# Optimization experiments

Hardware: AMD Instinct MI355X
Metric: run time of the kernel (lower is better)

Reference implementation:

```python
import jax, jax.numpy as jnp
import numpy as np
from jax import lax

# mamba-130m-style config
B, L = 2, 1024          # batch, seq_len
D = 768                 # hidden_size
E = 1536                # intermediate (expand=2)
N = 16                  # ssm state size
R = 48                  # time_step_rank = ceil(D/16)
K = 4                   # conv kernel
NL = 4                  # num layers
NC = 5                  # num classes
EPS = 1e-5


def setup_inputs() -> dict:
    key = jax.random.key(0)
    ks = jax.random.split(key, 10)
    s = 0.02
    return {
        "x": jax.random.normal(ks[0], (B, L, 12), dtype=jnp.float32),
        "proj_w": jax.random.normal(ks[1], (D, 12)) * s,
        "proj_b": jnp.zeros((D,), jnp.float32),
        "norm_w": jnp.ones((NL, D), jnp.float32),
        "in_w": jax.random.normal(ks[2], (NL, 2 * E, D)) * s,
        "conv_w": jax.random.normal(ks[3], (NL, E, K)) * s,
        "conv_b": jnp.zeros((NL, E), jnp.float32),
        "xproj_w": jax.random.normal(ks[4], (NL, R + 2 * N, E)) * s,
        "dt_w": jax.random.normal(ks[5], (NL, E, R)) * s,
        "dt_b": jnp.full((NL, E), -4.0, jnp.float32),  # softplus(-4) ~ small dt
        "A_log": jnp.tile(jnp.log(jnp.arange(1, N + 1, dtype=jnp.float32))[None, None, :], (NL, E, 1)),
        "D_param": jnp.ones((NL, E), jnp.float32),
        "out_w": jax.random.normal(ks[6], (NL, D, E)) * s,
        "fnorm_w": jnp.ones((D,), jnp.float32),
        "cls_w": jax.random.normal(ks[7], (NC, D)) * s,
        "cls_b": jnp.zeros((NC,), jnp.float32),
    }


def _rmsnorm(x, w):
    var = jnp.mean(x * x, axis=-1, keepdims=True)
    return x * lax.rsqrt(var + EPS) * w


def _causal_conv(u, w, b):
    # u: [B,L,E], w: [E,K] depthwise causal conv, left-pad K-1
    up = jnp.pad(u, ((0, 0), (K - 1, 0), (0, 0)))
    y = b
    for k in range(K):
        y = y + w[:, k] * up[:, k:k + L, :]
    return y


def _selective_scan(u, dt, A, Bm, Cm, Dp):
    # u, dt: [B,L,E]; Bm, Cm: [B,L,N]; A: [E,N]; Dp: [E]
    def step(h, inp):
        u_t, dt_t, B_t, C_t = inp  # [B,E],[B,E],[B,N],[B,N]
        dA = jnp.exp(dt_t[:, :, None] * A)                      # [B,E,N]
        h = h * dA + dt_t[:, :, None] * B_t[:, None, :] * u_t[:, :, None]
        y = jnp.einsum('ben,bn->be', h, C_t)
        return h, y

    h0 = jnp.zeros((u.shape[0], E, N), u.dtype)
    _, ys = lax.scan(step, h0,
                     (u.transpose(1, 0, 2), dt.transpose(1, 0, 2),
                      Bm.transpose(1, 0, 2), Cm.transpose(1, 0, 2)))
    return ys.transpose(1, 0, 2) + u * Dp


def reference(x, proj_w, proj_b, norm_w, in_w, conv_w, conv_b, xproj_w,
              dt_w, dt_b, A_log, D_param, out_w, fnorm_w, cls_w, cls_b):
    h = x @ proj_w.T + proj_b                                     # [B,L,D]
    for i in range(NL):
        res = h
        hn = _rmsnorm(h, norm_w[i])
        proj = hn @ in_w[i].T                                     # [B,L,2E]
        u, gate = proj[..., :E], proj[..., E:]
        u = jax.nn.silu(_causal_conv(u, conv_w[i], conv_b[i]))    # [B,L,E]
        xdbc = u @ xproj_w[i].T                                   # [B,L,R+2N]
        dt_r = xdbc[..., :R]
        Bm = xdbc[..., R:R + N]
        Cm = xdbc[..., R + N:]
        dt = jax.nn.softplus(dt_r @ dt_w[i].T + dt_b[i])          # [B,L,E]
        A = -jnp.exp(A_log[i])                                    # [E,N]
        y = _selective_scan(u, dt, A, Bm, Cm, D_param[i])
        y = y * jax.nn.silu(gate)
        h = res + y @ out_w[i].T
    h = _rmsnorm(h, fnorm_w)
    pooled = jnp.mean(h, axis=1)                                  # AdaptiveAvgPool1d(1)
    return pooled @ cls_w.T + cls_b                               # [B,NC]
```

## Files before the change

### kernel.cpp

```cpp
#include <hip/hip_runtime.h>

constexpr int B_  = 2;
constexpr int L_  = 1024;
constexpr int D_  = 768;
constexpr int E_  = 1536;
constexpr int N_  = 16;
constexpr int R_  = 48;
constexpr int NL_ = 4;
constexpr int NC_ = 5;
constexpr int M_  = B_ * L_;
constexpr int E2_ = 2 * E_;
constexpr int XD_ = R_ + 2 * N_;
constexpr float EPS_ = 1e-5f;

constexpr int NCH_ = 16;
constexpr int CL_  = L_ / NCH_;
constexpr int TS_  = 32;
constexpr int KS_  = 8;
constexpr int XSL_ = E_ / KS_;
constexpr int USTR_ = 200;

typedef __attribute__((ext_vector_type(8))) short bf16x8;
typedef __attribute__((ext_vector_type(4))) float f32x4;
typedef const __attribute__((address_space(1))) void* gas_t;
typedef __attribute__((address_space(3))) void* las_t;

__device__ __forceinline__ float sigm(float x) { return 1.0f / (1.0f + __expf(-x)); }
__device__ __forceinline__ float softplusf(float x) { return x > 20.0f ? x : log1pf(__expf(x)); }
__device__ __forceinline__ ushort f2b(float f) {
  union { float f; unsigned u; } v; v.f = f;
  unsigned r = (v.u + 0x7fffu + ((v.u >> 16) & 1u)) >> 16;
  return (ushort)r;
}
__device__ __forceinline__ float b2f(ushort u) {
  union { unsigned u; float f; } v; v.u = ((unsigned)u) << 16;
  return v.f;
}
__device__ __forceinline__ float b2f_lo(unsigned p) {
  union { unsigned u; float f; } v; v.u = p << 16;
  return v.f;
}
__device__ __forceinline__ float b2f_hi(unsigned p) {
  union { unsigned u; float f; } v; v.u = p & 0xffff0000u;
  return v.f;
}

template <int CTRL>
__device__ __forceinline__ float dpp_add(float x) {
  int yi = __builtin_amdgcn_update_dpp(0, __builtin_bit_cast(int, x), CTRL, 0xf, 0xf, false);
  return x + __builtin_bit_cast(float, yi);
}
__device__ __forceinline__ float row_sum16(float x) {
  x = dpp_add<0x121>(x);
  x = dpp_add<0x122>(x);
  x = dpp_add<0x124>(x);
  x = dpp_add<0x128>(x);
  return x;
}

__device__ __forceinline__ float block_sum(float v, float* sm) {
  #pragma unroll
  for (int o = 32; o > 0; o >>= 1) v += __shfl_xor(v, o);
  if ((threadIdx.x & 63) == 0) sm[threadIdx.x >> 6] = v;
  __syncthreads();
  return sm[0] + sm[1] + sm[2] + sm[3];
}

constexpr int WS1_ = NL_ * E2_ * D_;
constexpr int WS2_ = NL_ * D_ * E_;
constexpr int WS3_ = NL_ * XD_ * E_;
constexpr int WS4_ = NL_ * E_ * 64;
__global__ __launch_bounds__(256) void k_wprep(const float* __restrict__ in_w, const float* __restrict__ out_w,
                                               const float* __restrict__ xw, const float* __restrict__ dw,
                                               ushort* __restrict__ in_wb, ushort* __restrict__ out_wb,
                                               ushort* __restrict__ xwb, ushort* __restrict__ dtwb) {
  int i = (blockIdx.x * 256 + threadIdx.x) * 4;
  if (i < WS1_) {
    float4 v = *(const float4*)(in_w + i);
    *(ushort4*)(in_wb + i) = make_ushort4(f2b(v.x), f2b(v.y), f2b(v.z), f2b(v.w));
  } else if (i < WS1_ + WS2_) {
    int j = i - WS1_;
    float4 v = *(const float4*)(out_w + j);
    *(ushort4*)(out_wb + j) = make_ushort4(f2b(v.x), f2b(v.y), f2b(v.z), f2b(v.w));
  } else if (i < WS1_ + WS2_ + WS3_) {
    int j = i - WS1_ - WS2_;
    float4 v = *(const float4*)(xw + j);
    *(ushort4*)(xwb + j) = make_ushort4(f2b(v.x), f2b(v.y), f2b(v.z), f2b(v.w));
  } else if (i < WS1_ + WS2_ + WS3_ + WS4_) {
    int j = i - WS1_ - WS2_ - WS3_;
    int k = j & 63, e = j >> 6;
    ushort4 o;
    o.x = (k + 0 < R_) ? f2b(dw[e * R_ + k + 0]) : (ushort)0;
    o.y = (k + 1 < R_) ? f2b(dw[e * R_ + k + 1]) : (ushort)0;
    o.z = (k + 2 < R_) ? f2b(dw[e * R_ + k + 2]) : (ushort)0;
    o.w = (k + 3 < R_) ? f2b(dw[e * R_ + k + 3]) : (ushort)0;
    *(ushort4*)(dtwb + j) = o;
  }
}

__global__ __launch_bounds__(256) void k_proj(const float* __restrict__ x, const float* __restrict__ pw,
                                              const float* __restrict__ pb, float* __restrict__ h) {
  __shared__ float xs[12];
  int m = blockIdx.y;
  int d = blockIdx.x * 256 + threadIdx.x;
  if (threadIdx.x < 12) xs[threadIdx.x] = x[m * 12 + threadIdx.x];
  __syncthreads();
  float acc = pb[d];
  #pragma unroll
  for (int j = 0; j < 12; j++) acc = fmaf(xs[j], pw[d * 12 + j], acc);
  h[(size_t)m * D_ + d] = acc;
}

__global__ __launch_bounds__(256) void k_rmsnorm_bf(const float* __restrict__ h, const float* __restrict__ w,
                                                    ushort* __restrict__ hn) {
  __shared__ float sm[4];
  int m = blockIdx.x, tid = threadIdx.x;
  const float* row = h + (size_t)m * D_;
  float v0 = row[tid], v1 = row[tid + 256], v2 = row[tid + 512];
  float s = block_sum(v0 * v0 + v1 * v1 + v2 * v2, sm);
  float sc = rsqrtf(s * (1.0f / D_) + EPS_);
  ushort* o = hn + (size_t)m * D_;
  o[tid]       = f2b(v0 * sc * w[tid]);
  o[tid + 256] = f2b(v1 * sc * w[tid + 256]);
  o[tid + 512] = f2b(v2 * sc * w[tid + 512]);
}

template <int BM, int BN, int MODE>
__global__ __launch_bounds__(256) void k_gemm_bf(const ushort* __restrict__ A, const ushort* __restrict__ Bw,
                                                 void* __restrict__ Cv, const float* __restrict__ res,
                                                 int Kd, int Nd) {
  constexpr int AM = BM / 32, BNF = BN / 32;
  __shared__ ushort sA[BM * 32];
  __shared__ ushort sB[BN * 32];
  const int tid = threadIdx.x;
  const int wave = tid >> 6, lane = tid & 63;
  const int q = lane >> 4, r = lane & 15;
  const int wm = wave >> 1, wn = wave & 1;
  const int m0 = blockIdx.y * BM, n0 = blockIdx.x * BN;
  f32x4 acc[AM][BNF] = {};

  for (int k0 = 0; k0 < Kd; k0 += 32) {
    #pragma unroll
    for (int j = 0; j < BM / 64; j++) {
      int i = j * 256 + tid;
      const ushort* gp = A + (size_t)(m0 + (i >> 2)) * Kd + k0 + ((i & 3) << 3);
      __builtin_amdgcn_global_load_lds((gas_t)gp, (las_t)(sA + ((j * 256 + wave * 64) << 3)), 16, 0, 0);
    }
    #pragma unroll
    for (int j = 0; j < BN / 64; j++) {
      int i = j * 256 + tid;
      const ushort* gp = Bw + (size_t)(n0 + (i >> 2)) * Kd + k0 + ((i & 3) << 3);
      __builtin_amdgcn_global_load_lds((gas_t)gp, (las_t)(sB + ((j * 256 + wave * 64) << 3)), 16, 0, 0);
    }
    __syncthreads();
    bf16x8 af[AM], bfv[BNF];
    #pragma unroll
    for (int mi = 0; mi < AM; mi++)
      af[mi] = *(const bf16x8*)&sA[(wm * (BM / 2) + mi * 16 + r) * 32 + q * 8];
    #pragma unroll
    for (int nj = 0; nj < BNF; nj++)
      bfv[nj] = *(const bf16x8*)&sB[(wn * (BN / 2) + nj * 16 + r) * 32 + q * 8];
    #pragma unroll
    for (int mi = 0; mi < AM; mi++)
      #pragma unroll
      for (int nj = 0; nj < BNF; nj++)
        acc[mi][nj] = __builtin_amdgcn_mfma_f32_16x16x32_bf16(af[mi], bfv[nj], acc[mi][nj], 0, 0, 0);
    __syncthreads();
  }
  #pragma unroll
  for (int mi = 0; mi < AM; mi++) {
    #pragma unroll
    for (int nj = 0; nj < BNF; nj++) {
      int col = n0 + wn * (BN / 2) + nj * 16 + r;
      #pragma unroll
      for (int rg = 0; rg < 4; rg++) {
        int row = m0 + wm * (BM / 2) + mi * 16 + q * 4 + rg;
        size_t off = (size_t)row * Nd + col;
        float v = acc[mi][nj][rg];
        if (MODE == 4) {
          if (col >= (Nd >> 1)) v = v * sigm(v);
          ((ushort*)Cv)[off] = f2b(v);
        } else if (MODE == 6) {
          ((ushort*)Cv)[off] = f2b(softplusf(v + res[col]));
        } else {
          if (MODE == 1) v += res[off];
          ((float*)Cv)[off] = v;
        }
      }
    }
  }
}

__global__ __launch_bounds__(256) void k_gemm_xc(const ushort* __restrict__ proj, const float* __restrict__ cw,
                                                 const float* __restrict__ cb, const ushort* __restrict__ Bw,
                                                 ushort* __restrict__ ub16, float* __restrict__ part) {
  __shared__ ushort sU[64 * USTR_];
  __shared__ ushort sB[80 * USTR_];
  const int tid = threadIdx.x;
  const int wave = tid >> 6, lane = tid & 63;
  const int q = lane >> 4, r = lane & 15;
  const int m0 = blockIdx.x * 64;
  const int kbeg = blockIdx.y * XSL_;

  for (int i = tid; i < 80 * (XSL_ / 8); i += 256) {
    int row = i / (XSL_ / 8), seg = i % (XSL_ / 8);
    bf16x8 v = *(const bf16x8*)(Bw + (size_t)row * E_ + kbeg + seg * 8);
    *(bf16x8*)&sB[row * USTR_ + seg * 8] = v;
  }

  for (int i = tid; i < 64 * (XSL_ / 4); i += 256) {
    int row = i / (XSL_ / 4), e4i = i % (XSL_ / 4);
    int e = kbeg + e4i * 4;
    int m = m0 + row;
    int t = m & (L_ - 1);
    float4 w0 = *(const float4*)(cw + (e + 0) * 4);
    float4 w1 = *(const float4*)(cw + (e + 1) * 4);
    float4 w2 = *(const float4*)(cw + (e + 2) * 4);
    float4 w3 = *(const float4*)(cw + (e + 3) * 4);
    float wv[4][4] = {{w0.x, w0.y, w0.z, w0.w}, {w1.x, w1.y, w1.z, w1.w},
                      {w2.x, w2.y, w2.z, w2.w}, {w3.x, w3.y, w3.z, w3.w}};
    float4 bb = *(const float4*)(cb + e);
    float acc[4] = {bb.x, bb.y, bb.z, bb.w};
    #pragma unroll
    for (int k = 0; k < 4; k++) {
      int tt = t + k - 3;
      if (tt >= 0) {
        uint2 p = *(const uint2*)(proj + (size_t)(m + k - 3) * E2_ + e);
        acc[0] = fmaf(wv[0][k], b2f_lo(p.x), acc[0]);
        acc[1] = fmaf(wv[1][k], b2f_hi(p.x), acc[1]);
        acc[2] = fmaf(wv[2][k], b2f_lo(p.y), acc[2]);
        acc[3] = fmaf(wv[3][k], b2f_hi(p.y), acc[3]);
      }
    }
    float u0 = acc[0] * sigm(acc[0]), u1 = acc[1] * sigm(acc[1]);
    float u2 = acc[2] * sigm(acc[2]), u3 = acc[3] * sigm(acc[3]);
    uint2 uo;
    uo.x = (unsigned)f2b(u0) | ((unsigned)f2b(u1) << 16);
    uo.y = (unsigned)f2b(u2) | ((unsigned)f2b(u3) << 16);
    *(uint2*)(ub16 + (size_t)m * E_ + e) = uo;
    *(uint2*)&sU[row * USTR_ + e4i * 4] = uo;
  }
  __syncthreads();

  f32x4 acc[5] = {};
  #pragma unroll
  for (int k0 = 0; k0 < XSL_ / 32; k0++) {
    bf16x8 af = *(const bf16x8*)&sU[(wave * 16 + r) * USTR_ + k0 * 32 + q * 8];
    #pragma unroll
    for (int nj = 0; nj < 5; nj++) {
      bf16x8 bfv = *(const bf16x8*)&sB[(nj * 16 + r) * USTR_ + k0 * 32 + q * 8];
      acc[nj] = __builtin_amdgcn_mfma_f32_16x16x32_bf16(af, bfv, acc[nj], 0, 0, 0);
    }
  }
  float* pp = part + (size_t)blockIdx.y * M_ * XD_;
  #pragma unroll
  for (int nj = 0; nj < 5; nj++) {
    int col = nj * 16 + r;
    #pragma unroll
    for (int rg = 0; rg < 4; rg++) {
      int row = m0 + wave * 16 + q * 4 + rg;
      pp[(size_t)row * XD_ + col] = acc[nj][rg];
    }
  }
}

__global__ __launch_bounds__(256) void k_xfin(const float* __restrict__ part, float* __restrict__ xdbc,
                                              ushort* __restrict__ xb) {
  int i = blockIdx.x * 256 + threadIdx.x;
  int m = i / XD_, col = i - m * XD_;
  float s = 0.0f;
  #pragma unroll
  for (int ks = 0; ks < KS_; ks++) s += part[(size_t)ks * M_ * XD_ + i];
  xdbc[i] = s;
  if (col < R_) xb[(size_t)m * 64 + col] = f2b(s);
  else if (col < 64) xb[(size_t)m * 64 + col] = 0;
}

__global__ __launch_bounds__(256) void k_scanA(const ushort* __restrict__ u, const ushort* __restrict__ dtb,
                                               const float* __restrict__ xdbc, const float* __restrict__ A_log,
                                               float* __restrict__ Pst, float* __restrict__ Sst) {
  __shared__ float2 s_dtu[2][TS_][16];
  __shared__ float  s_b [2][TS_][16];
  const int tid = threadIdx.x;
  const int e0 = blockIdx.x << 4;
  const int b  = blockIdx.y;
  const int c  = blockIdx.z;
  const int n  = tid & 15, el = tid >> 4;
  const int e  = e0 + el;
  const float A = -__expf(A_log[e * N_ + n]);
  const int se = tid & 15, st = tid >> 4;

  float r_b[2];
  ushort r_dt[2], r_u[2];
  auto issue = [&](int s) {
    int t0 = c * CL_ + s * TS_;
    #pragma unroll
    for (int j = 0; j < 2; j++) {
      size_t m = (size_t)(b * L_ + t0 + j * 16 + st);
      r_dt[j] = dtb[m * E_ + e0 + se];
      r_u[j]  = u[m * E_ + e0 + se];
    }
    #pragma unroll
    for (int j = 0; j < 2; j++) {
      int idx = j * 256 + tid;
      r_b[j] = xdbc[(size_t)(b * L_ + t0 + (idx >> 4)) * XD_ + R_ + (idx & 15)];
    }
  };
  auto commit = [&](int pb) {
    #pragma unroll
    for (int j = 0; j < 2; j++) {
      int t = j * 16 + st;
      float dtv = b2f(r_dt[j]);
      s_dtu[pb][t][se] = make_float2(dtv, dtv * b2f(r_u[j]));
    }
    #pragma unroll
    for (int j = 0; j < 2; j++) {
      int idx = j * 256 + tid;
      s_b[pb][idx >> 4][idx & 15] = r_b[j];
    }
  };

  issue(0);
  commit(0);
  float hs = 0.0f, pp = 1.0f;
  constexpr int NS = CL_ / TS_;
  for (int s = 0; s < NS; s++) {
    __syncthreads();
    if (s + 1 < NS) issue(s + 1);
    const int pb = s & 1;
    #pragma unroll
    for (int t = 0; t < TS_; t++) {
      float2 dtu = s_dtu[pb][t][el];
      float bv   = s_b[pb][t][n];
      float dA = __expf(dtu.x * A);
      hs = fmaf(hs, dA, dtu.y * bv);
      pp *= dA;
    }
    if (s + 1 < NS) commit((s + 1) & 1);
  }
  size_t o = (((size_t)(b * NCH_ + c) * E_) + e) * N_ + n;
  Pst[o] = pp;
  Sst[o] = hs;
}

__global__ __launch_bounds__(256) void k_scanC(const ushort* __restrict__ u, const ushort* __restrict__ dtb,
                                               const float* __restrict__ xdbc, const ushort* __restrict__ proj,
                                               const float* __restrict__ A_log, const float* __restrict__ Dp,
                                               const float* __restrict__ Pst, const float* __restrict__ Sst,
                                               ushort* __restrict__ y) {
  __shared__ float2 s_dtu[2][TS_][16];
  __shared__ float2 s_bc [2][TS_][16];
  __shared__ float2 s_og [2][TS_][16];
  const int tid = threadIdx.x;
  const int e0 = blockIdx.x << 4;
  const int b  = blockIdx.y;
  const int c  = blockIdx.z;
  const int n  = tid & 15, el = tid >> 4;
  const int e  = e0 + el;
  const float A = -__expf(A_log[e * N_ + n]);
  const int se = tid & 15, st = tid >> 4;
  const float Dv = Dp[e0 + se];

  float r_bc[4];
  ushort r_dt[2], r_u[2], r_g[2];
  auto issue = [&](int s) {
    int t0 = c * CL_ + s * TS_;
    #pragma unroll
    for (int j = 0; j < 2; j++) {
      size_t m = (size_t)(b * L_ + t0 + j * 16 + st);
      r_dt[j] = dtb[m * E_ + e0 + se];
      r_u[j]  = u[m * E_ + e0 + se];
      r_g[j]  = proj[m * E2_ + E_ + e0 + se];
    }
    #pragma unroll
    for (int j = 0; j < 4; j++) {
      int idx = j * 256 + tid;
      r_bc[j] = xdbc[(size_t)(b * L_ + t0 + (idx >> 5)) * XD_ + R_ + (idx & 31)];
    }
  };
  auto commit = [&](int pb) {
    #pragma unroll
    for (int j = 0; j < 2; j++) {
      int t = j * 16 + st;
      float dtv = b2f(r_dt[j]);
      float uf = b2f(r_u[j]);
      s_dtu[pb][t][se] = make_float2(dtv, dtv * uf);
      s_og[pb][t][se] = make_float2(uf * Dv, b2f(r_g[j]));
    }
    #pragma unroll
    for (int j = 0; j < 4; j++) {
      int idx = j * 256 + tid;
      int t = idx >> 5, col = idx & 31;
      ((float*)&s_bc[pb][t][0])[((col & 15) << 1) + (col >> 4)] = r_bc[j];
    }
  };

  issue(0);
  float hs = 0.0f;
  for (int cc = 0; cc < c; cc++) {
    size_t o = (((size_t)(b * NCH_ + cc) * E_) + e) * N_ + n;
    hs = fmaf(Pst[o], hs, Sst[o]);
  }
  commit(0);
  constexpr int NS = CL_ / TS_;
  for (int s = 0; s < NS; s++) {
    __syncthreads();
    if (s + 1 < NS) issue(s + 1);
    const int pb = s & 1;
    const int mbase = b * L_ + c * CL_ + s * TS_;
    #pragma unroll
    for (int t = 0; t < TS_; t++) {
      float2 dtu = s_dtu[pb][t][el];
      float2 bc  = s_bc[pb][t][n];
      float dA = __expf(dtu.x * A);
      hs = fmaf(hs, dA, dtu.y * bc.x);
      float p = row_sum16(hs * bc.y);
      if (n == 0) {
        float2 og = s_og[pb][t][el];
        y[(size_t)(mbase + t) * E_ + e] = f2b((p + og.x) * og.y);
      }
    }
    if (s + 1 < NS) commit((s + 1) & 1);
  }
}

__global__ __launch_bounds__(256) void k_rowscale(const float* __restrict__ h, float* __restrict__ rs) {
  __shared__ float sm[4];
  int m = blockIdx.x, tid = threadIdx.x;
  const float* row = h + (size_t)m * D_;
  float v0 = row[tid], v1 = row[tid + 256], v2 = row[tid + 512];
  float s = block_sum(v0 * v0 + v1 * v1 + v2 * v2, sm);
  if (tid == 0) rs[m] = rsqrtf(s * (1.0f / D_) + EPS_);
}

__global__ __launch_bounds__(256) void k_pool(const float* __restrict__ h, const float* __restrict__ rs,
                                              const float* __restrict__ fw, float* __restrict__ pooled) {
  int d = blockIdx.x * 256 + threadIdx.x;
  int t0 = blockIdx.y * 128;
  int b = blockIdx.z;
  float acc = 0.0f;
  for (int t = t0; t < t0 + 128; t++) {
    int m = b * L_ + t;
    acc = fmaf(h[(size_t)m * D_ + d], rs[m], acc);
  }
  atomicAdd(&pooled[b * D_ + d], acc * fw[d] * (1.0f / L_));
}

__global__ __launch_bounds__(256) void k_logits(const float* __restrict__ pooled, const float* __restrict__ cw,
                                                const float* __restrict__ cb, float* __restrict__ out) {
  int wv = threadIdx.x >> 6, ln = threadIdx.x & 63;
  for (int p = wv; p < B_ * NC_; p += 4) {
    int b = p / NC_, c = p % NC_;
    float s = 0.0f;
    for (int d = ln; d < D_; d += 64) s = fmaf(pooled[b * D_ + d], cw[c * D_ + d], s);
    #pragma unroll
    for (int o = 32; o > 0; o >>= 1) s += __shfl_xor(s, o);
    if (ln == 0) out[p] = s + cb[c];
  }
}

extern "C" void kernel_launch(void* const* d_in, const int* in_sizes, int n_in,
                              void* d_out, int out_size, void* d_ws, size_t ws_size,
                              hipStream_t stream) {
  const float* x       = (const float*)d_in[0];
  const float* proj_w  = (const float*)d_in[1];
  const float* proj_b  = (const float*)d_in[2];
  const float* norm_w  = (const float*)d_in[3];
  const float* in_w    = (const float*)d_in[4];
  const float* conv_w  = (const float*)d_in[5];
  const float* conv_b  = (const float*)d_in[6];
  const float* xproj_w = (const float*)d_in[7];
  const float* dt_w    = (const float*)d_in[8];
  const float* dt_b    = (const float*)d_in[9];
  const float* A_log   = (const float*)d_in[10];
  const float* D_param = (const float*)d_in[11];
  const float* out_w   = (const float*)d_in[12];
  const float* fnorm_w = (const float*)d_in[13];
  const float* cls_w   = (const float*)d_in[14];
  const float* cls_b   = (const float*)d_in[15];
  float* out = (float*)d_out;

  float* h      = (float*)d_ws;
  float* xdbc   = h + (size_t)M_ * D_;
  float* rsb    = xdbc + (size_t)M_ * XD_;
  float* pooled = rsb + M_;
  float* Pst    = pooled + B_ * D_;
  float* Sst    = Pst + (size_t)B_ * NCH_ * E_ * N_;
  float* xpart  = Sst + (size_t)B_ * NCH_ * E_ * N_;
  ushort* proj_bf = (ushort*)(xpart + (size_t)KS_ * M_ * XD_);
  ushort* hn_bf   = proj_bf + (size_t)M_ * E2_;
  ushort* y_bf    = hn_bf + (size_t)M_ * D_;
  ushort* ub_bf   = y_bf + (size_t)M_ * E_;
  ushort* dt_bf   = ub_bf + (size_t)M_ * E_;
  ushort* xdbc_bf = dt_bf + (size_t)M_ * E_;
  ushort* xwb     = xdbc_bf + (size_t)M_ * 64;
  ushort* dtwb    = xwb + (size_t)NL_ * XD_ * E_;
  ushort* in_wb   = dtwb + (size_t)NL_ * E_ * 64;
  ushort* out_wb  = in_wb + (size_t)NL_ * E2_ * D_;

  constexpr int WTOT = WS1_ + WS2_ + WS3_ + WS4_;
  k_wprep<<<(WTOT / 4 + 255) / 256, 256, 0, stream>>>(in_w, out_w, xproj_w, dt_w,
                                                      in_wb, out_wb, xwb, dtwb);

  k_proj<<<dim3(D_ / 256, M_), 256, 0, stream>>>(x, proj_w, proj_b, h);

  for (int i = 0; i < NL_; i++) {
    k_rmsnorm_bf<<<M_, 256, 0, stream>>>(h, norm_w + i * D_, hn_bf);
    k_gemm_bf<64, 128, 4><<<dim3(E2_ / 128, M_ / 64), 256, 0, stream>>>(
        hn_bf, in_wb + (size_t)i * E2_ * D_, proj_bf, nullptr, D_, E2_);
    k_gemm_xc<<<dim3(M_ / 64, KS_), 256, 0, stream>>>(proj_bf, conv_w + i * E_ * 4, conv_b + i * E_,
                                                      xwb + (size_t)i * XD_ * E_, ub_bf, xpart);
    k_xfin<<<M_ * XD_ / 256, 256, 0, stream>>>(xpart, xdbc, xdbc_bf);
    k_gemm_bf<64, 64, 6><<<dim3(E_ / 64, M_ / 64), 256, 0, stream>>>(
        xdbc_bf, dtwb + (size_t)i * E_ * 64, dt_bf, dt_b + i * E_, 64, E_);
    k_scanA<<<dim3(E_ / 16, B_, NCH_), 256, 0, stream>>>(ub_bf, dt_bf, xdbc,
                                                         A_log + (size_t)i * E_ * N_, Pst, Sst);
    k_scanC<<<dim3(E_ / 16, B_, NCH_), 256, 0, stream>>>(ub_bf, dt_bf, xdbc, proj_bf,
                                                         A_log + (size_t)i * E_ * N_, D_param + i * E_,
                                                         Pst, Sst, y_bf);
    k_gemm_bf<64, 64, 1><<<dim3(D_ / 64, M_ / 64), 256, 0, stream>>>(
        y_bf, out_wb + (size_t)i * D_ * E_, h, h, E_, D_);
  }

  k_rowscale<<<M_, 256, 0, stream>>>(h, rsb);
  hipMemsetAsync(pooled, 0, (size_t)B_ * D_ * sizeof(float), stream);
  k_pool<<<dim3(D_ / 256, L_ / 128, B_), 256, 0, stream>>>(h, rsb, fnorm_w, pooled);
  k_logits<<<1, 256, 0, stream>>>(pooled, cls_w, cls_b, out);
}
```

Before: 715.8 us.

## Split in-proj output into u/gate buffers and load whole scan chunks at once

The in-projection GEMM now writes u and silu(gate) into two separate contiguous [M,E] bf16 buffers instead of one interleaved [M,2E] buffer, so the conv and scan kernels read denser rows. The scan kernels drop their double-buffered 32-step staging and load the full 64-step chunk into shared memory up front, with an occupancy hint of 6 blocks. scanC also preloads all prior chunk carry states with unrolled loads instead of a serial dependent loop, and stages y in shared memory so it can store coalesced 8-byte rows. The cost is more shared memory and registers per block, and no overlap between loading and the recurrence.

New measurement: 707.9 us. About the same (-1.1%).

```diff
diff --git a/kernel.cpp b/kernel.cpp
--- a/kernel.cpp
+++ b/kernel.cpp
@@ -15,7 +15,6 @@
 
 constexpr int NCH_ = 16;
 constexpr int CL_  = L_ / NCH_;
-constexpr int TS_  = 32;
 constexpr int KS_  = 8;
 constexpr int XSL_ = E_ / KS_;
 constexpr int USTR_ = 200;
@@ -128,7 +127,7 @@
 template <int BM, int BN, int MODE>
 __global__ __launch_bounds__(256) void k_gemm_bf(const ushort* __restrict__ A, const ushort* __restrict__ Bw,
                                                  void* __restrict__ Cv, const float* __restrict__ res,
-                                                 int Kd, int Nd) {
+                                                 void* __restrict__ Cv2, int Kd, int Nd) {
   constexpr int AM = BM / 32, BNF = BN / 32;
   __shared__ ushort sA[BM * 32];
   __shared__ ushort sB[BN * 32];
@@ -175,14 +174,18 @@
       #pragma unroll
       for (int rg = 0; rg < 4; rg++) {
         int row = m0 + wm * (BM / 2) + mi * 16 + q * 4 + rg;
-        size_t off = (size_t)row * Nd + col;
         float v = acc[mi][nj][rg];
         if (MODE == 4) {
-          if (col >= (Nd >> 1)) v = v * sigm(v);
-          ((ushort*)Cv)[off] = f2b(v);
+          if (col >= E_) {
+            v = v * sigm(v);
+            ((ushort*)Cv2)[(size_t)row * E_ + col - E_] = f2b(v);
+          } else {
+            ((ushort*)Cv)[(size_t)row * E_ + col] = f2b(v);
+          }
         } else if (MODE == 6) {
-          ((ushort*)Cv)[off] = f2b(softplusf(v + res[col]));
+          ((ushort*)Cv)[(size_t)row * Nd + col] = f2b(softplusf(v + res[col]));
         } else {
+          size_t off = (size_t)row * Nd + col;
           if (MODE == 1) v += res[off];
           ((float*)Cv)[off] = v;
         }
@@ -191,7 +194,7 @@
   }
 }
 
-__global__ __launch_bounds__(256) void k_gemm_xc(const ushort* __restrict__ proj, const float* __restrict__ cw,
+__global__ __launch_bounds__(256) void k_gemm_xc(const ushort* __restrict__ proju, const float* __restrict__ cw,
                                                  const float* __restrict__ cb, const ushort* __restrict__ Bw,
                                                  ushort* __restrict__ ub16, float* __restrict__ part) {
   __shared__ ushort sU[64 * USTR_];
@@ -225,7 +228,7 @@
     for (int k = 0; k < 4; k++) {
       int tt = t + k - 3;
       if (tt >= 0) {
-        uint2 p = *(const uint2*)(proj + (size_t)(m + k - 3) * E2_ + e);
+        uint2 p = *(const uint2*)(proju + (size_t)(m + k - 3) * E_ + e);
         acc[0] = fmaf(wv[0][k], b2f_lo(p.x), acc[0]);
         acc[1] = fmaf(wv[1][k], b2f_hi(p.x), acc[1]);
         acc[2] = fmaf(wv[2][k], b2f_lo(p.y), acc[2]);
@@ -276,11 +279,11 @@
   else if (col < 64) xb[(size_t)m * 64 + col] = 0;
 }
 
-__global__ __launch_bounds__(256) void k_scanA(const ushort* __restrict__ u, const ushort* __restrict__ dtb,
-                                               const float* __restrict__ xdbc, const float* __restrict__ A_log,
-                                               float* __restrict__ Pst, float* __restrict__ Sst) {
-  __shared__ float2 s_dtu[2][TS_][16];
-  __shared__ float  s_b [2][TS_][16];
+__global__ __launch_bounds__(256, 6) void k_scanA(const ushort* __restrict__ u, const ushort* __restrict__ dtb,
+                                                  const float* __restrict__ xdbc, const float* __restrict__ A_log,
+                                                  float* __restrict__ Pst, float* __restrict__ Sst) {
+  __shared__ float2 s_dtu[CL_][16];
+  __shared__ float  s_b [CL_][16];
   const int tid = threadIdx.x;
   const int e0 = blockIdx.x << 4;
   const int b  = blockIdx.y;
@@ -288,69 +291,50 @@
   const int n  = tid & 15, el = tid >> 4;
   const int e  = e0 + el;
   const float A = -__expf(A_log[e * N_ + n]);
-  const int se = tid & 15, st = tid >> 4;
-
-  float r_b[2];
-  ushort r_dt[2], r_u[2];
-  auto issue = [&](int s) {
-    int t0 = c * CL_ + s * TS_;
-    #pragma unroll
-    for (int j = 0; j < 2; j++) {
-      size_t m = (size_t)(b * L_ + t0 + j * 16 + st);
-      r_dt[j] = dtb[m * E_ + e0 + se];
-      r_u[j]  = u[m * E_ + e0 + se];
-    }
-    #pragma unroll
-    for (int j = 0; j < 2; j++) {
-      int idx = j * 256 + tid;
-      r_b[j] = xdbc[(size_t)(b * L_ + t0 + (idx >> 4)) * XD_ + R_ + (idx & 15)];
-    }
-  };
-  auto commit = [&](int pb) {
-    #pragma unroll
-    for (int j = 0; j < 2; j++) {
-      int t = j * 16 + st;
-      float dtv = b2f(r_dt[j]);
-      s_dtu[pb][t][se] = make_float2(dtv, dtv * b2f(r_u[j]));
-    }
-    #pragma unroll
-    for (int j = 0; j < 2; j++) {
-      int idx = j * 256 + tid;
-      s_b[pb][idx >> 4][idx & 15] = r_b[j];
-    }
-  };
-
-  issue(0);
-  commit(0);
+  const int t0 = c * CL_;
+
+  ushort r_dt[4], r_u[4];
+  float r_b[4];
+  #pragma unroll
+  for (int j = 0; j < 4; j++) {
+    size_t m = (size_t)(b * L_ + t0 + j * 16 + el);
+    r_dt[j] = dtb[m * E_ + e0 + n];
+    r_u[j]  = u[m * E_ + e0 + n];
+    int idx = j * 256 + tid;
+    r_b[j] = xdbc[(size_t)(b * L_ + t0 + (idx >> 4)) * XD_ + R_ + (idx & 15)];
+  }
+  #pragma unroll
+  for (int j = 0; j < 4; j++) {
+    int t = j * 16 + el;
+    float dtv = b2f(r_dt[j]);
+    s_dtu[t][n] = make_float2(dtv, dtv * b2f(r_u[j]));
+    int idx = j * 256 + tid;
+    s_b[idx >> 4][idx & 15] = r_b[j];
+  }
+  __syncthreads();
+
   float hs = 0.0f, pp = 1.0f;
-  constexpr int NS = CL_ / TS_;
-  for (int s = 0; s < NS; s++) {
-    __syncthreads();
-    if (s + 1 < NS) issue(s + 1);
-    const int pb = s & 1;
-    #pragma unroll
-    for (int t = 0; t < TS_; t++) {
-      float2 dtu = s_dtu[pb][t][el];
-      float bv   = s_b[pb][t][n];
-      float dA = __expf(dtu.x * A);
-      hs = fmaf(hs, dA, dtu.y * bv);
-      pp *= dA;
-    }
-    if (s + 1 < NS) commit((s + 1) & 1);
+  #pragma unroll 8
+  for (int t = 0; t < CL_; t++) {
+    float2 dtu = s_dtu[t][el];
+    float dA = __expf(dtu.x * A);
+    hs = fmaf(hs, dA, dtu.y * s_b[t][n]);
+    pp *= dA;
   }
   size_t o = (((size_t)(b * NCH_ + c) * E_) + e) * N_ + n;
   Pst[o] = pp;
   Sst[o] = hs;
 }
 
-__global__ __launch_bounds__(256) void k_scanC(const ushort* __restrict__ u, const ushort* __restrict__ dtb,
-                                               const float* __restrict__ xdbc, const ushort* __restrict__ proj,
-                                               const float* __restrict__ A_log, const float* __restrict__ Dp,
-                                               const float* __restrict__ Pst, const float* __restrict__ Sst,
-                                               ushort* __restrict__ y) {
-  __shared__ float2 s_dtu[2][TS_][16];
-  __shared__ float2 s_bc [2][TS_][16];
-  __shared__ float2 s_og [2][TS_][16];
+__global__ __launch_bounds__(256, 6) void k_scanC(const ushort* __restrict__ u, const ushort* __restrict__ dtb,
+                                                  const float* __restrict__ xdbc, const ushort* __restrict__ gb,
+                                                  const float* __restrict__ A_log, const float* __restrict__ Dp,
+                                                  const float* __restrict__ Pst, const float* __restrict__ Sst,
+                                                  ushort* __restrict__ y) {
+  __shared__ float2 s_dtu[CL_][16];
+  __shared__ float2 s_bc [CL_][16];
+  __shared__ float2 s_og [CL_][16];
+  __shared__ ushort s_y [CL_][16];
   const int tid = threadIdx.x;
   const int e0 = blockIdx.x << 4;
   const int b  = blockIdx.y;
@@ -358,69 +342,75 @@
   const int n  = tid & 15, el = tid >> 4;
   const int e  = e0 + el;
   const float A = -__expf(A_log[e * N_ + n]);
-  const int se = tid & 15, st = tid >> 4;
-  const float Dv = Dp[e0 + se];
-
-  float r_bc[4];
-  ushort r_dt[2], r_u[2], r_g[2];
-  auto issue = [&](int s) {
-    int t0 = c * CL_ + s * TS_;
-    #pragma unroll
-    for (int j = 0; j < 2; j++) {
-      size_t m = (size_t)(b * L_ + t0 + j * 16 + st);
-      r_dt[j] = dtb[m * E_ + e0 + se];
-      r_u[j]  = u[m * E_ + e0 + se];
-      r_g[j]  = proj[m * E2_ + E_ + e0 + se];
-    }
-    #pragma unroll
-    for (int j = 0; j < 4; j++) {
-      int idx = j * 256 + tid;
-      r_bc[j] = xdbc[(size_t)(b * L_ + t0 + (idx >> 5)) * XD_ + R_ + (idx & 31)];
-    }
-  };
-  auto commit = [&](int pb) {
-    #pragma unroll
-    for (int j = 0; j < 2; j++) {
-      int t = j * 16 + st;
-      float dtv = b2f(r_dt[j]);
-      float uf = b2f(r_u[j]);
-      s_dtu[pb][t][se] = make_float2(dtv, dtv * uf);
-      s_og[pb][t][se] = make_float2(uf * Dv, b2f(r_g[j]));
-    }
-    #pragma unroll
-    for (int j = 0; j < 4; j++) {
-      int idx = j * 256 + tid;
-      int t = idx >> 5, col = idx & 31;
-      ((float*)&s_bc[pb][t][0])[((col & 15) << 1) + (col >> 4)] = r_bc[j];
-    }
-  };
-
-  issue(0);
+  const float Dv = Dp[e0 + n];
+  const int t0 = c * CL_;
+
+  ushort r_dt[4], r_u[4], r_g[4];
+  float r_bc[8];
+  #pragma unroll
+  for (int j = 0; j < 4; j++) {
+    size_t m = (size_t)(b * L_ + t0 + j * 16 + el);
+    r_dt[j] = dtb[m * E_ + e0 + n];
+    r_u[j]  = u[m * E_ + e0 + n];
+    r_g[j]  = gb[m * E_ + e0 + n];
+  }
+  #pragma unroll
+  for (int j = 0; j < 8; j++) {
+    int idx = j * 256 + tid;
+    r_bc[j] = xdbc[(size_t)(b * L_ + t0 + (idx >> 5)) * XD_ + R_ + (idx & 31)];
+  }
+
   float hs = 0.0f;
-  for (int cc = 0; cc < c; cc++) {
-    size_t o = (((size_t)(b * NCH_ + cc) * E_) + e) * N_ + n;
-    hs = fmaf(Pst[o], hs, Sst[o]);
-  }
-  commit(0);
-  constexpr int NS = CL_ / TS_;
-  for (int s = 0; s < NS; s++) {
-    __syncthreads();
-    if (s + 1 < NS) issue(s + 1);
-    const int pb = s & 1;
-    const int mbase = b * L_ + c * CL_ + s * TS_;
-    #pragma unroll
-    for (int t = 0; t < TS_; t++) {
-      float2 dtu = s_dtu[pb][t][el];
-      float2 bc  = s_bc[pb][t][n];
-      float dA = __expf(dtu.x * A);
-      hs = fmaf(hs, dA, dtu.y * bc.x);
-      float p = row_sum16(hs * bc.y);
-      if (n == 0) {
-        float2 og = s_og[pb][t][el];
-        y[(size_t)(mbase + t) * E_ + e] = f2b((p + og.x) * og.y);
-      }
-    }
-    if (s + 1 < NS) commit((s + 1) & 1);
+  if (c > 0) {
+    float pv[NCH_ - 1], sv[NCH_ - 1];
+    #pragma unroll
+    for (int cc = 0; cc < NCH_ - 1; cc++) {
+      int ci = cc < c ? cc : c - 1;
+      size_t o = (((size_t)(b * NCH_ + ci) * E_) + e) * N_ + n;
+      pv[cc] = Pst[o];
+      sv[cc] = Sst[o];
+    }
+    #pragma unroll
+    for (int cc = 0; cc < NCH_ - 1; cc++) {
+      bool v = cc < c;
+      hs = fmaf(v ? pv[cc] : 1.0f, hs, v ? sv[cc] : 0.0f);
+    }
+  }
+
+  #pragma unroll
+  for (int j = 0; j < 4; j++) {
+    int t = j * 16 + el;
+    float dtv = b2f(r_dt[j]);
+    float uf = b2f(r_u[j]);
+    s_dtu[t][n] = make_float2(dtv, dtv * uf);
+    s_og[t][n] = make_float2(uf * Dv, b2f(r_g[j]));
+  }
+  #pragma unroll
+  for (int j = 0; j < 8; j++) {
+    int idx = j * 256 + tid;
+    int t = idx >> 5, col = idx & 31;
+    ((float*)&s_bc[t][0])[((col & 15) << 1) + (col >> 4)] = r_bc[j];
+  }
+  __syncthreads();
+
+  #pragma unroll 8
+  for (int t = 0; t < CL_; t++) {
+    float2 dtu = s_dtu[t][el];
+    float2 bc  = s_bc[t][n];
+    float dA = __expf(dtu.x * A);
+    hs = fmaf(hs, dA, dtu.y * bc.x);
+    float p = row_sum16(hs * bc.y);
+    if (n == 0) {
+      float2 og = s_og[t][el];
+      s_y[t][el] = f2b((p + og.x) * og.y);
+    }
+  }
+  __syncthreads();
+
+  {
+    int row = tid >> 2, seg = tid & 3;
+    uint2 v = *(const uint2*)&s_y[row][seg * 4];
+    *(uint2*)(y + (size_t)(b * L_ + t0 + row) * E_ + e0 + seg * 4) = v;
   }
 }
 
@@ -487,8 +477,9 @@
   float* Pst    = pooled + B_ * D_;
   float* Sst    = Pst + (size_t)B_ * NCH_ * E_ * N_;
   float* xpart  = Sst + (size_t)B_ * NCH_ * E_ * N_;
-  ushort* proj_bf = (ushort*)(xpart + (size_t)KS_ * M_ * XD_);
-  ushort* hn_bf   = proj_bf + (size_t)M_ * E2_;
+  ushort* proju_bf = (ushort*)(xpart + (size_t)KS_ * M_ * XD_);
+  ushort* g_bf    = proju_bf + (size_t)M_ * E_;
+  ushort* hn_bf   = g_bf + (size_t)M_ * E_;
   ushort* y_bf    = hn_bf + (size_t)M_ * D_;
   ushort* ub_bf   = y_bf + (size_t)M_ * E_;
   ushort* dt_bf   = ub_bf + (size_t)M_ * E_;
@@ -507,19 +498,19 @@
   for (int i = 0; i < NL_; i++) {
     k_rmsnorm_bf<<<M_, 256, 0, stream>>>(h, norm_w + i * D_, hn_bf);
     k_gemm_bf<64, 128, 4><<<dim3(E2_ / 128, M_ / 64), 256, 0, stream>>>(
-        hn_bf, in_wb + (size_t)i * E2_ * D_, proj_bf, nullptr, D_, E2_);
-    k_gemm_xc<<<dim3(M_ / 64, KS_), 256, 0, stream>>>(proj_bf, conv_w + i * E_ * 4, conv_b + i * E_,
+        hn_bf, in_wb + (size_t)i * E2_ * D_, proju_bf, nullptr, g_bf, D_, E2_);
+    k_gemm_xc<<<dim3(M_ / 64, KS_), 256, 0, stream>>>(proju_bf, conv_w + i * E_ * 4, conv_b + i * E_,
                                                       xwb + (size_t)i * XD_ * E_, ub_bf, xpart);
     k_xfin<<<M_ * XD_ / 256, 256, 0, stream>>>(xpart, xdbc, xdbc_bf);
     k_gemm_bf<64, 64, 6><<<dim3(E_ / 64, M_ / 64), 256, 0, stream>>>(
-        xdbc_bf, dtwb + (size_t)i * E_ * 64, dt_bf, dt_b + i * E_, 64, E_);
+        xdbc_bf, dtwb + (size_t)i * E_ * 64, dt_bf, dt_b + i * E_, nullptr, 64, E_);
     k_scanA<<<dim3(E_ / 16, B_, NCH_), 256, 0, stream>>>(ub_bf, dt_bf, xdbc,
                                                          A_log + (size_t)i * E_ * N_, Pst, Sst);
-    k_scanC<<<dim3(E_ / 16, B_, NCH_), 256, 0, stream>>>(ub_bf, dt_bf, xdbc, proj_bf,
+    k_scanC<<<dim3(E_ / 16, B_, NCH_), 256, 0, stream>>>(ub_bf, dt_bf, xdbc, g_bf,
                                                          A_log + (size_t)i * E_ * N_, D_param + i * E_,
                                                          Pst, Sst, y_bf);
     k_gemm_bf<64, 64, 1><<<dim3(D_ / 64, M_ / 64), 256, 0, stream>>>(
-        y_bf, out_wb + (size_t)i * D_ * E_, h, h, E_, D_);
+        y_bf, out_wb + (size_t)i * D_ * E_, h, h, nullptr, E_, D_);
   }
 
   k_rowscale<<<M_, 256, 0, stream>>>(h, rsb);
```
